# Kernel tuning notes

Measured on AMD Instinct MI355X. Metric: run time of the kernel, lower is better.

The kernel has to match this reference:

```python
import jax, jax.numpy as jnp
import numpy as np

IGNORE = 255
THRESH = 0.7
MIN_KEPT = 100000
AUX_W = 1.0


def resize_bilinear_ac(x, oh, ow):
    # F.interpolate(..., mode='bilinear', align_corners=True); x: (b,c,h,w)
    b, c, h, w = x.shape
    ys = jnp.linspace(0.0, h - 1.0, oh)
    xs = jnp.linspace(0.0, w - 1.0, ow)
    y0 = jnp.floor(ys).astype(jnp.int32)
    x0 = jnp.floor(xs).astype(jnp.int32)
    y1 = jnp.minimum(y0 + 1, h - 1)
    x1 = jnp.minimum(x0 + 1, w - 1)
    wy = (ys - y0)[:, None]          # (oh,1) broadcasts over (b,c,oh,w)
    wx = xs - x0                     # (ow,)
    rows = x[:, :, y0, :] * (1.0 - wy) + x[:, :, y1, :] * wy   # (b,c,oh,w)
    return rows[:, :, :, x0] * (1.0 - wx) + rows[:, :, :, x1] * wx


def ohem_ce(pred, target):
    # pred: (b,c,h,w) logits, target: (b,h,w) int labels
    b, c, h, w = pred.shape
    n = b * h * w
    t = target.reshape(-1)
    valid = t != IGNORE
    t_cl = jnp.where(valid, t, 0)
    logits = pred.transpose(0, 2, 3, 1).reshape(n, c)
    logp = jax.nn.log_softmax(logits, axis=-1)
    pix = jnp.arange(n)
    logp_t = logp[pix, t_cl]
    # prob at target class; invalid pixels filled with 1 (as in masked_fill_)
    mask_prob = jnp.where(valid, jnp.exp(logp_t), 1.0)
    idx = min(n, MIN_KEPT) - 1
    thr = jnp.maximum(jnp.asarray(THRESH, pred.dtype), jnp.sort(mask_prob)[idx])
    kept = mask_prob <= thr
    final_valid = valid & kept
    nll = -logp_t
    denom = jnp.maximum(final_valid.sum(), 1).astype(pred.dtype)
    return jnp.sum(jnp.where(final_valid, nll, 0.0)) / denom


def boundary_bce(p, t):
    # p: (n,1,h,w) probs, t: (n,1,h,w) binary targets; per-sample pos/neg weights
    pos = jnp.sum(t == 1.0, axis=(1, 2, 3), keepdims=True).astype(p.dtype)
    neg = jnp.sum(t == 0.0, axis=(1, 2, 3), keepdims=True).astype(p.dtype)
    valid = pos + neg
    wgt = jnp.where(t == 1.0, neg / valid, jnp.where(t == 0.0, pos / valid, 0.0))
    logp = jnp.clip(jnp.log(p), -100.0)          # torch BCELoss clamps log at -100
    log1mp = jnp.clip(jnp.log(1.0 - p), -100.0)
    bce = -(t * logp + (1.0 - t) * log1mp)
    return jnp.mean(wgt * bce)


def setup_inputs() -> dict:
    key = jax.random.key(0)
    k1, k2, k3, k4, k5 = jax.random.split(key, 5)
    main_pred = jax.random.normal(k1, (4, 19, 64, 128), dtype=jnp.float32)
    coarse_pred = jax.random.normal(k2, (4, 19, 64, 128), dtype=jnp.float32)
    boundary_pred = jax.random.uniform(k3, (4, 1, 64, 128), dtype=jnp.float32)
    seg_gt = jax.random.randint(k4, (4, 512, 1024), 0, 19, dtype=jnp.int32)
    boundary_gt = jax.random.randint(k5, (4, 1, 512, 1024), 0, 2).astype(jnp.float32)
    return {"main_pred": main_pred, "coarse_pred": coarse_pred,
            "boundary_pred": boundary_pred, "seg_gt": seg_gt,
            "boundary_gt": boundary_gt}


def reference(main_pred, coarse_pred, boundary_pred, seg_gt, boundary_gt):
    h, w = seg_gt.shape[1], seg_gt.shape[2]
    main_up = resize_bilinear_ac(main_pred, h, w)
    loss = ohem_ce(main_up, seg_gt)
    coarse_up = resize_bilinear_ac(coarse_pred, h, w)
    loss = loss + AUX_W * ohem_ce(coarse_up, seg_gt)
    bound_up = resize_bilinear_ac(boundary_pred, h, w)
    loss = loss + boundary_bce(bound_up, boundary_gt)
    return loss
```

## Files before the change

### kernel.cpp

```cpp
#include <hip/hip_runtime.h>

#define NPX    2097152
#define NPX4   (NPX/4)
#define CH_STR 8192
#define IMG_STR 155648

#define OFF_CTL   (2ull*NPX*4)
#define CTL_HIST    0
#define CTL_CNT1    0
#define CTL_CNT2    2048
#define CTL_BAR     24576
#define CTL_FLAG    24579
#define CTL_PREFIX  24580
#define CTL_KREM    24582
#define CTL_THR     24584
#define CTL_PPSUM   24586
#define CTL_PPCNT   28682
#define CTL_OPSUM   32778
#define CTL_OPCNT   33290
#define CTL_BPS     33802
#define CTL_BPC     34826

#define MAGIC_FAST 0x3A9C67E5u
#define GRID_P1    4608u

__device__ __forceinline__ void st_dev_f(float* p, float v) {
    __hip_atomic_store(p, v, __ATOMIC_RELAXED, __HIP_MEMORY_SCOPE_AGENT);
}
__device__ __forceinline__ void st_dev_u(unsigned* p, unsigned v) {
    __hip_atomic_store(p, v, __ATOMIC_RELAXED, __HIP_MEMORY_SCOPE_AGENT);
}
__device__ __forceinline__ float ld_dev_f(const float* p) {
    return __hip_atomic_load((float*)p, __ATOMIC_RELAXED, __HIP_MEMORY_SCOPE_AGENT);
}
__device__ __forceinline__ unsigned ld_dev_u(const unsigned* p) {
    return __hip_atomic_load((unsigned*)p, __ATOMIC_RELAXED, __HIP_MEMORY_SCOPE_AGENT);
}

__global__ __launch_bounds__(256) void fused_pass1(
    const float* __restrict__ mp, const float* __restrict__ cp,
    const float* __restrict__ bp, const int* __restrict__ seg,
    const float* __restrict__ bg,
    float* __restrict__ probA, float* __restrict__ ppsum, unsigned* __restrict__ ppcnt,
    float* __restrict__ bps, unsigned* __restrict__ bpc,
    unsigned* __restrict__ cnt1, unsigned* __restrict__ cnt2,
    unsigned* __restrict__ flag,
    float* __restrict__ out)
{
    __shared__ float2 erow[19 * 128];
    __shared__ float rf[4]; __shared__ unsigned ru[4];
    __shared__ float rf2[4]; __shared__ unsigned ru2[4];
    __shared__ unsigned amLast;
    __shared__ float Pb[4], Nb[4]; __shared__ unsigned PCb[4], NCb[4];
    int bk = blockIdx.x;
    int tid = threadIdx.x;

    if (bk < 4096) {
        int x = bk & 7, j = bk >> 3;
        int v = ((j >> 3) << 6) | (x << 3) | (j & 7);
        int head = v >> 11;
        int task = v & 2047;
        int b = task >> 9;
        int y = task & 511;
        const float* pred = head ? cp : mp;

        float fy = (float)y * (63.0f / 511.0f);
        int y0 = min((int)fy, 63);
        int y1 = min(y0 + 1, 63);
        float wy = fy - (float)y0;

        const float* r0 = pred + (size_t)b * IMG_STR + y0 * 128;
        const float* r1 = pred + (size_t)b * IMG_STR + y1 * 128;
        for (int i = tid; i < 2432; i += 256) {
            int c = i >> 7, xx = i & 127;
            float v0 = r0[c * CH_STR + xx];
            float v1 = r1[c * CH_STR + xx];
            float e = fmaf(wy, v1 - v0, v0);
            erow[c * 128 + xx].x = e;
            if (xx > 0)    erow[c * 128 + xx - 1].y = e;
            if (xx == 127) erow[c * 128 + 127].y = e;
        }
        __syncthreads();

        int xb = tid << 2;
        int P = (b * 512 + y) * 1024 + xb;
        int4 t4 = *(const int4*)(seg + P);
        int t[4] = {t4.x, t4.y, t4.z, t4.w};

        float fx0 = (float)xb * (127.0f / 1023.0f);
        int X = min((int)fx0, 126);
        float wA[4], wB[4], wC[4];
#pragma unroll
        for (int dx = 0; dx < 4; ++dx) {
            float fx = (float)(xb + dx) * (127.0f / 1023.0f);
            int x0 = min((int)fx, 127);
            float wx = fx - (float)x0;
            bool sm = (x0 == X);
            wA[dx] = sm ? (1.0f - wx) : 0.0f;
            wB[dx] = sm ? wx : (1.0f - wx);
            wC[dx] = sm ? 0.0f : wx;
        }

        float s[4] = {0.f, 0.f, 0.f, 0.f};
        for (int c = 0; c < 19; ++c) {
            float2 eA = erow[c * 128 + X];
            float2 eB = erow[c * 128 + X + 1];
#pragma unroll
            for (int dx = 0; dx < 4; ++dx) {
                float l = fmaf(eA.x, wA[dx], fmaf(eA.y, wB[dx], eB.y * wC[dx]));
                s[dx] += __expf(l);
            }
        }

        float fs = 0.f; unsigned ic = 0;
        float pr[4];
#pragma unroll
        for (int dx = 0; dx < 4; ++dx) {
            bool valid = (t[dx] != 255);
            int tc = valid ? t[dx] : 0;
            float2 eA = erow[tc * 128 + X];
            float2 eB = erow[tc * 128 + X + 1];
            float lt = fmaf(eA.x, wA[dx], fmaf(eA.y, wB[dx], eB.y * wC[dx]));
            float ls = __logf(s[dx]);
            float n  = ls - lt;
            float p  = fminf(__expf(-n), 1.0f);
            pr[dx] = valid ? p : 1.0f;
            if (valid && p <= 0.7f) { fs += n; ic++; }
        }
        *(float4*)(probA + (size_t)head * NPX + P) = make_float4(pr[0], pr[1], pr[2], pr[3]);

        for (int o = 32; o; o >>= 1) {
            fs += __shfl_down(fs, o, 64);
            ic += (unsigned)__shfl_down((int)ic, o, 64);
        }
        int wave = tid >> 6, lane = tid & 63;
        if (lane == 0) { rf[wave] = fs; ru[wave] = ic; }
        __syncthreads();
        if (tid == 0) {
            st_dev_f(&ppsum[head * 2048 + task], rf[0] + rf[1] + rf[2] + rf[3]);
            st_dev_u(&ppcnt[head * 2048 + task], ru[0] + ru[1] + ru[2] + ru[3]);
        }
    } else {
        int bb = bk - 4096;
        int b  = bb >> 7;
        int blk = bb & 127;
        float psum = 0.f, nsum = 0.f; unsigned pc = 0, nc = 0;

        for (int g = blk * 256 + tid; g < 131072; g += 128 * 256) {
            int P = g << 2;
            int y = P >> 10, xb = P & 1023;

            float fy = (float)y * (63.0f / 511.0f);
            int y0 = min((int)fy, 63);
            int y1 = min(y0 + 1, 63);
            float wy = fy - (float)y0;

            const float* r0 = bp + b * 8192 + y0 * 128;
            const float* r1 = bp + b * 8192 + y1 * 128;
            float fx0 = (float)xb * (127.0f / 1023.0f);
            int X  = min((int)fx0, 126);
            int X2 = min(X + 2, 127);
            float c0 = r0[X], c1 = r0[X + 1], c2 = r0[X2];
            float d0 = r1[X], d1 = r1[X + 1], d2 = r1[X2];
            float e0 = fmaf(wy, d0 - c0, c0);
            float e1 = fmaf(wy, d1 - c1, c1);
            float e2 = fmaf(wy, d2 - c2, c2);

            float4 t4 = *(const float4*)(bg + (size_t)b * 524288 + P);
            float tv[4] = {t4.x, t4.y, t4.z, t4.w};

#pragma unroll
            for (int dx = 0; dx < 4; ++dx) {
                float fx = (float)(xb + dx) * (127.0f / 1023.0f);
                int x0 = min((int)fx, 127);
                int x1 = min(x0 + 1, 127);
                float wx = fx - (float)x0;
                float a0 = (x0 == X)     ? e0 : e1;
                float a1 = (x1 == X + 1) ? e1 : e2;
                float p  = fmaf(wx, a1 - a0, a0);
                bool isp = (tv[dx] == 1.0f);
                bool isn = (tv[dx] == 0.0f);
                float q = isp ? p : 1.0f - p;
                float l = fmaxf(__logf(q), -100.0f);
                if (isp) { pc++; psum -= l; }
                if (isn) { nc++; nsum -= l; }
            }
        }
        for (int o = 32; o; o >>= 1) {
            psum += __shfl_down(psum, o, 64);
            nsum += __shfl_down(nsum, o, 64);
            pc   += (unsigned)__shfl_down((int)pc, o, 64);
            nc   += (unsigned)__shfl_down((int)nc, o, 64);
        }
        int wave = tid >> 6, lane = tid & 63;
        if (lane == 0) { rf[wave] = psum; rf2[wave] = nsum; ru[wave] = pc; ru2[wave] = nc; }
        __syncthreads();
        if (tid == 0) {
            st_dev_f(&bps[2 * bb],     rf[0] + rf[1] + rf[2] + rf[3]);
            st_dev_f(&bps[2 * bb + 1], rf2[0] + rf2[1] + rf2[2] + rf2[3]);
            st_dev_u(&bpc[2 * bb],     ru[0] + ru[1] + ru[2] + ru[3]);
            st_dev_u(&bpc[2 * bb + 1], ru2[0] + ru2[1] + ru2[2] + ru2[3]);
        }
    }

    __syncthreads();
    if (tid == 0) {
        asm volatile("s_waitcnt vmcnt(0)" ::: "memory");
        unsigned last = 0u;
        unsigned o1 = __hip_atomic_fetch_add(&cnt1[(bk & 63) << 5], 1u,
                                             __ATOMIC_RELAXED, __HIP_MEMORY_SCOPE_AGENT);
        if (o1 == 71u) {
            unsigned o2 = __hip_atomic_fetch_add(cnt2, 1u,
                                                 __ATOMIC_RELAXED, __HIP_MEMORY_SCOPE_AGENT);
            last = (o2 == 63u) ? 1u : 0u;
        }
        amLast = last;
    }
    __syncthreads();
    if (!amLast) return;

    float s0 = 0.f, s1 = 0.f; unsigned c0 = 0u, c1 = 0u;
    for (int i = tid; i < 2048; i += 256) {
        s0 += ld_dev_f(&ppsum[i]);        c0 += ld_dev_u(&ppcnt[i]);
        s1 += ld_dev_f(&ppsum[2048 + i]); c1 += ld_dev_u(&ppcnt[2048 + i]);
    }
    for (int o = 32; o; o >>= 1) {
        s0 += __shfl_down(s0, o, 64); s1 += __shfl_down(s1, o, 64);
        c0 += (unsigned)__shfl_down((int)c0, o, 64);
        c1 += (unsigned)__shfl_down((int)c1, o, 64);
    }
    int wv = tid >> 6, ln = tid & 63;
    if (ln == 0) { rf[wv] = s0; rf2[wv] = s1; ru[wv] = c0; ru2[wv] = c1; }
    __syncthreads();
    float S0 = rf[0] + rf[1] + rf[2] + rf[3];
    float S1 = rf2[0] + rf2[1] + rf2[2] + rf2[3];
    unsigned C0 = ru[0] + ru[1] + ru[2] + ru[3];
    unsigned C1 = ru2[0] + ru2[1] + ru2[2] + ru2[3];
    bool fast = (C0 >= 100000u) && (C1 >= 100000u);

    if (fast) {
        float*    lf = (float*)erow;
        unsigned* lu = (unsigned*)erow + 256;
        for (int b = 0; b < 4; ++b) {
            float ps = 0.f, ns = 0.f; unsigned p_c = 0, n_c = 0;
            if (tid < 128) {
                int jj = b * 128 + tid;
                ps  = ld_dev_f(&bps[2 * jj]); ns  = ld_dev_f(&bps[2 * jj + 1]);
                p_c = ld_dev_u(&bpc[2 * jj]); n_c = ld_dev_u(&bpc[2 * jj + 1]);
            }
            lf[tid] = ps; lu[tid] = p_c; __syncthreads();
            for (int o = 128; o; o >>= 1) {
                if (tid < o) { lf[tid] += lf[tid + o]; lu[tid] += lu[tid + o]; }
                __syncthreads();
            }
            if (tid == 0) { Pb[b] = lf[0]; PCb[b] = lu[0]; }
            __syncthreads();
            lf[tid] = ns; lu[tid] = n_c; __syncthreads();
            for (int o = 128; o; o >>= 1) {
                if (tid < o) { lf[tid] += lf[tid + o]; lu[tid] += lu[tid + o]; }
                __syncthreads();
            }
            if (tid == 0) { Nb[b] = lf[0]; NCb[b] = lu[0]; }
            __syncthreads();
        }
        if (tid == 0) {
            float bt = 0.f;
            for (int b = 0; b < 4; ++b) {
                float pos = (float)PCb[b], neg = (float)NCb[b];
                float val = fmaxf(pos + neg, 1.f);
                bt += (neg / val) * Pb[b] + (pos / val) * Nb[b];
            }
            float hls = S0 / fmaxf((float)C0, 1.f) + S1 / fmaxf((float)C1, 1.f);
            out[0] = hls + bt / 2097152.0f;
            st_dev_u(flag, MAGIC_FAST);
        }
    }
}

__device__ __forceinline__ void gbar(unsigned* bar, int tid) {
    __syncthreads();
    if (tid == 0) {
        unsigned g = __hip_atomic_load(&bar[1], __ATOMIC_RELAXED, __HIP_MEMORY_SCOPE_AGENT);
        unsigned t = __hip_atomic_fetch_add(&bar[0], 1u, __ATOMIC_ACQ_REL, __HIP_MEMORY_SCOPE_AGENT);
        if (t == 255u) {
            __hip_atomic_store(&bar[0], 0u, __ATOMIC_RELAXED, __HIP_MEMORY_SCOPE_AGENT);
            __hip_atomic_store(&bar[1], g + 1u, __ATOMIC_RELEASE, __HIP_MEMORY_SCOPE_AGENT);
        } else {
            while (__hip_atomic_load(&bar[1], __ATOMIC_ACQUIRE, __HIP_MEMORY_SCOPE_AGENT) == g)
                __builtin_amdgcn_s_sleep(8);
        }
    }
    __syncthreads();
}

__device__ void combine_out(int tid, float headLossSum,
                            const float* __restrict__ bps, const unsigned* __restrict__ bpc,
                            float* __restrict__ out)
{
    __shared__ float lf[256]; __shared__ unsigned lu[256];
    __shared__ float Pb[4], Nb[4]; __shared__ unsigned PCb[4], NCb[4];
    for (int b = 0; b < 4; ++b) {
        float ps = 0.f, ns = 0.f; unsigned p_c = 0, n_c = 0;
        if (tid < 128) {
            int j = b * 128 + tid;
            ps = bps[2 * j]; ns = bps[2 * j + 1];
            p_c = bpc[2 * j]; n_c = bpc[2 * j + 1];
        }
        lf[tid] = ps; lu[tid] = p_c; __syncthreads();
        for (int o = 128; o; o >>= 1) {
            if (tid < o) { lf[tid] += lf[tid + o]; lu[tid] += lu[tid + o]; }
            __syncthreads();
        }
        if (tid == 0) { Pb[b] = lf[0]; PCb[b] = lu[0]; }
        __syncthreads();
        lf[tid] = ns; lu[tid] = n_c; __syncthreads();
        for (int o = 128; o; o >>= 1) {
            if (tid < o) { lf[tid] += lf[tid + o]; lu[tid] += lu[tid + o]; }
            __syncthreads();
        }
        if (tid == 0) { Nb[b] = lf[0]; NCb[b] = lu[0]; }
        __syncthreads();
    }
    if (tid == 0) {
        float bt = 0.f;
        for (int b = 0; b < 4; ++b) {
            float pos = (float)PCb[b], neg = (float)NCb[b];
            float val = fmaxf(pos + neg, 1.f);
            bt += (neg / val) * Pb[b] + (pos / val) * Nb[b];
        }
        out[0] = headLossSum + bt / 2097152.0f;
    }
}

__global__ __launch_bounds__(256) void finish_all(
    const float* __restrict__ probA, const int* __restrict__ seg,
    const float* __restrict__ ppsum, const unsigned* __restrict__ ppcnt,
    const float* __restrict__ bps, const unsigned* __restrict__ bpc,
    unsigned* __restrict__ hist, unsigned* __restrict__ bar,
    unsigned* __restrict__ prefix, unsigned* __restrict__ krem,
    float* __restrict__ thr,
    float* __restrict__ opsum, unsigned* __restrict__ opcnt,
    unsigned* __restrict__ flag,
    float* __restrict__ out)
{
    if (*flag == MAGIC_FAST)
        return;

    int tid = threadIdx.x, blk = blockIdx.x;
    int wave = tid >> 6, lane = tid & 63;

    float s0 = 0.f, s1 = 0.f; unsigned c0 = 0u, c1 = 0u;
    for (int i = tid; i < 2048; i += 256) {
        s0 += ppsum[i];        c0 += ppcnt[i];
        s1 += ppsum[2048 + i]; c1 += ppcnt[2048 + i];
    }
    for (int o = 32; o; o >>= 1) {
        s0 += __shfl_down(s0, o, 64); s1 += __shfl_down(s1, o, 64);
        c0 += (unsigned)__shfl_down((int)c0, o, 64);
        c1 += (unsigned)__shfl_down((int)c1, o, 64);
    }
    __shared__ float ws0[4], ws1[4]; __shared__ unsigned wc0[4], wc1[4];
    if (lane == 0) { ws0[wave] = s0; ws1[wave] = s1; wc0[wave] = c0; wc1[wave] = c1; }
    __syncthreads();
    float S0 = ws0[0] + ws0[1] + ws0[2] + ws0[3];
    float S1 = ws1[0] + ws1[1] + ws1[2] + ws1[3];
    unsigned C0 = wc0[0] + wc0[1] + wc0[2] + wc0[3];
    unsigned C1 = wc1[0] + wc1[1] + wc1[2] + wc1[3];
    bool done0 = C0 >= 100000u, done1 = C1 >= 100000u;

    if (done0 && done1) {
        if (blk == 0)
            combine_out(tid, S0 / fmaxf((float)C0, 1.f) + S1 / fmaxf((float)C1, 1.f),
                        bps, bpc, out);
        return;
    }

    __shared__ unsigned hsh[4096];
    __shared__ unsigned cpre[257];
    unsigned doneMask = (done0 ? 1u : 0u) | (done1 ? 2u : 0u);

    for (int i = blk * 256 + tid; i < 24576; i += 65536) hist[i] = 0u;
    gbar(bar, tid);

    for (int lvl = 0; lvl < 3; ++lvl) {
        unsigned* hl = hist + lvl * 8192;
        for (int h = 0; h < 2; ++h) {
            if (doneMask & (1u << h)) continue;
            unsigned pre = (lvl == 0) ? 0u : prefix[h];
            for (int i = tid; i < 4096; i += 256) hsh[i] = 0u;
            __syncthreads();
            const float4* prob = (const float4*)(probA + (size_t)h * NPX);
            for (int i = blk * 256 + tid; i < NPX4; i += 65536) {
                float4 p = prob[i];
                unsigned u[4] = {__float_as_uint(p.x), __float_as_uint(p.y),
                                 __float_as_uint(p.z), __float_as_uint(p.w)};
#pragma unroll
                for (int k = 0; k < 4; ++k) {
                    unsigned bv = u[k];
                    if (lvl == 0)      atomicAdd(&hsh[bv >> 18], 1u);
                    else if (lvl == 1) { if ((bv >> 18) == pre) atomicAdd(&hsh[(bv >> 6) & 0xFFFu], 1u); }
                    else               { if ((bv >> 6) == pre) atomicAdd(&hsh[bv & 63u], 1u); }
                }
            }
            __syncthreads();
            for (int i = tid; i < 4096; i += 256) {
                unsigned v = hsh[i];
                if (v) atomicAdd(&hl[h * 4096 + i], v);
            }
            __syncthreads();
        }
        gbar(bar, tid);
        if (blk == 0) {
            int bins = (lvl == 2) ? 64 : 4096;
            for (int h = 0; h < 2; ++h) {
                if (doneMask & (1u << h)) continue;
                const unsigned* hh = hl + h * 4096;
                int per = (bins + 255) >> 8;
                int base = tid * per;
                unsigned ssum = 0;
                for (int i = 0; i < per; ++i) { int idx = base + i; if (idx < bins) ssum += hh[idx]; }
                cpre[tid] = ssum; __syncthreads();
                if (tid == 0) {
                    unsigned acc = 0;
                    for (int i = 0; i < 256; ++i) { unsigned v = cpre[i]; cpre[i] = acc; acc += v; }
                    cpre[256] = acc;
                }
                __syncthreads();
                unsigned K = (lvl == 0) ? 100000u : krem[h];
                unsigned my = cpre[tid], nx = cpre[tid + 1];
                if (K > 0 && my < K && K <= nx) {
                    unsigned acc = my;
                    for (int i = 0; i < per; ++i) {
                        int idx = base + i;
                        unsigned c = (idx < bins) ? hh[idx] : 0u;
                        if (acc < K && K <= acc + c) {
                            if (lvl == 0)      { prefix[h] = (unsigned)idx; krem[h] = K - acc; }
                            else if (lvl == 1) { prefix[h] = (prefix[h] << 12) | (unsigned)idx; krem[h] = K - acc; }
                            else {
                                unsigned bitsv = (prefix[h] << 6) | (unsigned)idx;
                                thr[h] = fmaxf(0.7f, __uint_as_float(bitsv));
                            }
                            break;
                        }
                        acc += c;
                    }
                }
                __syncthreads();
            }
        }
        gbar(bar, tid);
    }

    for (int h = 0; h < 2; ++h) {
        if (doneMask & (1u << h)) continue;
        float th = thr[h];
        const float4* prob = (const float4*)(probA + (size_t)h * NPX);
        const int4*   sg4  = (const int4*)seg;
        float fs = 0.f; unsigned ic = 0;
        for (int i = blk * 256 + tid; i < NPX4; i += 65536) {
            float4 p = prob[i]; int4 tt = sg4[i];
            if (tt.x != 255 && p.x <= th) { fs -= __logf(p.x); ic++; }
            if (tt.y != 255 && p.y <= th) { fs -= __logf(p.y); ic++; }
            if (tt.z != 255 && p.z <= th) { fs -= __logf(p.z); ic++; }
            if (tt.w != 255 && p.w <= th) { fs -= __logf(p.w); ic++; }
        }
        for (int o = 32; o; o >>= 1) {
            fs += __shfl_down(fs, o, 64);
            ic += (unsigned)__shfl_down((int)ic, o, 64);
        }
        __shared__ float wf[4]; __shared__ unsigned wu[4];
        if (lane == 0) { wf[wave] = fs; wu[wave] = ic; }
        __syncthreads();
        if (tid == 0) {
            opsum[h * 256 + blk] = wf[0] + wf[1] + wf[2] + wf[3];
            opcnt[h * 256 + blk] = wu[0] + wu[1] + wu[2] + wu[3];
        }
        __syncthreads();
    }
    gbar(bar, tid);
    if (blk == 0) {
        __shared__ float lf2[256]; __shared__ unsigned lu2[256];
        float hls = 0.f;
        for (int h = 0; h < 2; ++h) {
            float S; unsigned C;
            if (doneMask & (1u << h)) {
                S = h ? S1 : S0; C = h ? C1 : C0;
            } else {
                lf2[tid] = opsum[h * 256 + tid]; lu2[tid] = opcnt[h * 256 + tid];
                __syncthreads();
                for (int o = 128; o; o >>= 1) {
                    if (tid < o) { lf2[tid] += lf2[tid + o]; lu2[tid] += lu2[tid + o]; }
                    __syncthreads();
                }
                S = lf2[0]; C = lu2[0];
                __syncthreads();
            }
            hls += S / fmaxf((float)C, 1.f);
        }
        combine_out(tid, hls, bps, bpc, out);
    }
}

extern "C" void kernel_launch(void* const* d_in, const int* in_sizes, int n_in,
                              void* d_out, int out_size, void* d_ws, size_t ws_size,
                              hipStream_t stream)
{
    const float* mp  = (const float*)d_in[0];
    const float* cp  = (const float*)d_in[1];
    const float* bp  = (const float*)d_in[2];
    const int*   seg = (const int*)d_in[3];
    const float* bg  = (const float*)d_in[4];
    float* out = (float*)d_out;

    char* ws = (char*)d_ws;
    float* probA = (float*)ws;
    unsigned* ctl    = (unsigned*)(ws + OFF_CTL);
    unsigned* hist   = ctl + CTL_HIST;
    unsigned* cnt1   = ctl + CTL_CNT1;
    unsigned* cnt2   = ctl + CTL_CNT2;
    unsigned* bar    = ctl + CTL_BAR;
    unsigned* flag   = ctl + CTL_FLAG;
    unsigned* prefix = ctl + CTL_PREFIX;
    unsigned* krem   = ctl + CTL_KREM;
    float*    thr    = (float*)(ctl + CTL_THR);
    float*    ppsum  = (float*)(ctl + CTL_PPSUM);
    unsigned* ppcnt  = ctl + CTL_PPCNT;
    float*    opsum  = (float*)(ctl + CTL_OPSUM);
    unsigned* opcnt  = ctl + CTL_OPCNT;
    float*    bps    = (float*)(ctl + CTL_BPS);
    unsigned* bpc    = ctl + CTL_BPC;

    hipMemsetAsync(ws + OFF_CTL, 0, 24580ull * 4, stream);

    fused_pass1<<<dim3(GRID_P1), 256, 0, stream>>>(mp, cp, bp, seg, bg, probA,
                                                   ppsum, ppcnt, bps, bpc,
                                                   cnt1, cnt2, flag, out);
    finish_all<<<dim3(256), 256, 0, stream>>>(probA, seg, ppsum, ppcnt, bps, bpc,
                                              hist, bar, prefix, krem, thr,
                                              opsum, opcnt, flag, out);
}
```

Baseline: 113.3 us.

## Process four output rows per block, reusing three loaded source rows in registers

Each segmentation block now handles four consecutive output rows instead of one. It loads the three source rows those rows can span once into registers as float4 vectors, then builds the per-row interpolated shared buffer with shuffles and vector stores. This cuts redundant global loads of source rows and block launch overhead, and shrinks the pass-1 grid, so the last-block counter threshold is adjusted to match. The cost is more registers (launch bounds now request 5 blocks), fewer blocks in flight, and extra syncthreads per row.

Result: no change. 113.1 us (-0.2%).

```diff
diff --git a/kernel.cpp b/kernel.cpp
--- a/kernel.cpp
+++ b/kernel.cpp
@@ -22,7 +22,7 @@
 #define CTL_BPC     34826
 
 #define MAGIC_FAST 0x3A9C67E5u
-#define GRID_P1    4608u
+#define GRID_P1    1536u
 
 __device__ __forceinline__ void st_dev_f(float* p, float v) {
     __hip_atomic_store(p, v, __ATOMIC_RELAXED, __HIP_MEMORY_SCOPE_AGENT);
@@ -37,7 +37,7 @@
     return __hip_atomic_load((unsigned*)p, __ATOMIC_RELAXED, __HIP_MEMORY_SCOPE_AGENT);
 }
 
-__global__ __launch_bounds__(256) void fused_pass1(
+__global__ __launch_bounds__(256, 5) void fused_pass1(
     const float* __restrict__ mp, const float* __restrict__ cp,
     const float* __restrict__ bp, const int* __restrict__ seg,
     const float* __restrict__ bg,
@@ -55,38 +55,34 @@
     int bk = blockIdx.x;
     int tid = threadIdx.x;
 
-    if (bk < 4096) {
-        int x = bk & 7, j = bk >> 3;
-        int v = ((j >> 3) << 6) | (x << 3) | (j & 7);
-        int head = v >> 11;
-        int task = v & 2047;
-        int b = task >> 9;
-        int y = task & 511;
+    if (bk < 1024) {
+        int v = ((bk & 7) << 7) | (bk >> 3);
+        int head = v >> 9;
+        int b    = (v >> 7) & 3;
+        int k    = v & 127;
         const float* pred = head ? cp : mp;
 
-        float fy = (float)y * (63.0f / 511.0f);
-        int y0 = min((int)fy, 63);
-        int y1 = min(y0 + 1, 63);
-        float wy = fy - (float)y0;
-
-        const float* r0 = pred + (size_t)b * IMG_STR + y0 * 128;
-        const float* r1 = pred + (size_t)b * IMG_STR + y1 * 128;
-        for (int i = tid; i < 2432; i += 256) {
-            int c = i >> 7, xx = i & 127;
-            float v0 = r0[c * CH_STR + xx];
-            float v1 = r1[c * CH_STR + xx];
-            float e = fmaf(wy, v1 - v0, v0);
-            erow[c * 128 + xx].x = e;
-            if (xx > 0)    erow[c * 128 + xx - 1].y = e;
-            if (xx == 127) erow[c * 128 + 127].y = e;
-        }
-        __syncthreads();
+        int y0g = min((int)((float)(4 * k) * (63.0f / 511.0f)), 63);
+        int row0 = y0g, row1 = min(y0g + 1, 63), row2 = min(y0g + 2, 63);
+
+        float4 rv[3][3];
+#pragma unroll
+        for (int r = 0; r < 3; ++r) {
+            int ry = (r == 0) ? row0 : ((r == 1) ? row1 : row2);
+            const float* rp = pred + (size_t)b * IMG_STR + ry * 128;
+#pragma unroll
+            for (int sr = 0; sr < 3; ++sr) {
+                int s = tid + (sr << 8);
+                if (s < 608) {
+                    int c = s >> 5, x4 = (s & 31) << 2;
+                    rv[r][sr] = *(const float4*)(rp + c * CH_STR + x4);
+                } else {
+                    rv[r][sr] = make_float4(0.f, 0.f, 0.f, 0.f);
+                }
+            }
+        }
 
         int xb = tid << 2;
-        int P = (b * 512 + y) * 1024 + xb;
-        int4 t4 = *(const int4*)(seg + P);
-        int t[4] = {t4.x, t4.y, t4.z, t4.w};
-
         float fx0 = (float)xb * (127.0f / 1023.0f);
         int X = min((int)fx0, 126);
         float wA[4], wB[4], wC[4];
@@ -101,47 +97,82 @@
             wC[dx] = sm ? 0.0f : wx;
         }
 
-        float s[4] = {0.f, 0.f, 0.f, 0.f};
-        for (int c = 0; c < 19; ++c) {
-            float2 eA = erow[c * 128 + X];
-            float2 eB = erow[c * 128 + X + 1];
+#pragma unroll 1
+        for (int d = 0; d < 4; ++d) {
+            int y = (k << 2) + d;
+            int task = (b << 9) + y;
+            float fy = (float)y * (63.0f / 511.0f);
+            int y0 = min((int)fy, 63);
+            float wy = fy - (float)y0;
+            int j = y0 - y0g;
+
+            int P = task * 1024 + xb;
+            int4 t4 = *(const int4*)(seg + P);
+            int t[4] = {t4.x, t4.y, t4.z, t4.w};
+
+#pragma unroll
+            for (int sr = 0; sr < 3; ++sr) {
+                int s = tid + (sr << 8);
+                float4 cu = (j == 0) ? rv[0][sr] : rv[1][sr];
+                float4 nx = (j == 0) ? rv[1][sr] : rv[2][sr];
+                float e0 = fmaf(wy, nx.x - cu.x, cu.x);
+                float e1 = fmaf(wy, nx.y - cu.y, cu.y);
+                float e2 = fmaf(wy, nx.z - cu.z, cu.z);
+                float e3 = fmaf(wy, nx.w - cu.w, cu.w);
+                float en = __shfl_down(e0, 1, 64);
+                if (s < 608) {
+                    int c = s >> 5, x4 = (s & 31) << 2;
+                    float last = ((s & 31) == 31) ? e3 : en;
+                    float4 w0 = make_float4(e0, e1, e1, e2);
+                    float4 w1 = make_float4(e2, e3, e3, last);
+                    *(float4*)(&erow[c * 128 + x4])     = w0;
+                    *(float4*)(&erow[c * 128 + x4 + 2]) = w1;
+                }
+            }
+            __syncthreads();
+
+            float acc[4] = {0.f, 0.f, 0.f, 0.f};
+            for (int c = 0; c < 19; ++c) {
+                float2 eA = erow[c * 128 + X];
+                float2 eB = erow[c * 128 + X + 1];
+#pragma unroll
+                for (int dx = 0; dx < 4; ++dx) {
+                    float l = fmaf(eA.x, wA[dx], fmaf(eA.y, wB[dx], eB.y * wC[dx]));
+                    acc[dx] += __expf(l);
+                }
+            }
+
+            float fs = 0.f; unsigned ic = 0;
+            float pr[4];
 #pragma unroll
             for (int dx = 0; dx < 4; ++dx) {
-                float l = fmaf(eA.x, wA[dx], fmaf(eA.y, wB[dx], eB.y * wC[dx]));
-                s[dx] += __expf(l);
-            }
-        }
-
-        float fs = 0.f; unsigned ic = 0;
-        float pr[4];
-#pragma unroll
-        for (int dx = 0; dx < 4; ++dx) {
-            bool valid = (t[dx] != 255);
-            int tc = valid ? t[dx] : 0;
-            float2 eA = erow[tc * 128 + X];
-            float2 eB = erow[tc * 128 + X + 1];
-            float lt = fmaf(eA.x, wA[dx], fmaf(eA.y, wB[dx], eB.y * wC[dx]));
-            float ls = __logf(s[dx]);
-            float n  = ls - lt;
-            float p  = fminf(__expf(-n), 1.0f);
-            pr[dx] = valid ? p : 1.0f;
-            if (valid && p <= 0.7f) { fs += n; ic++; }
-        }
-        *(float4*)(probA + (size_t)head * NPX + P) = make_float4(pr[0], pr[1], pr[2], pr[3]);
-
-        for (int o = 32; o; o >>= 1) {
-            fs += __shfl_down(fs, o, 64);
-            ic += (unsigned)__shfl_down((int)ic, o, 64);
-        }
-        int wave = tid >> 6, lane = tid & 63;
-        if (lane == 0) { rf[wave] = fs; ru[wave] = ic; }
-        __syncthreads();
-        if (tid == 0) {
-            st_dev_f(&ppsum[head * 2048 + task], rf[0] + rf[1] + rf[2] + rf[3]);
-            st_dev_u(&ppcnt[head * 2048 + task], ru[0] + ru[1] + ru[2] + ru[3]);
+                bool valid = (t[dx] != 255);
+                int tc = valid ? t[dx] : 0;
+                float2 eA = erow[tc * 128 + X];
+                float2 eB = erow[tc * 128 + X + 1];
+                float lt = fmaf(eA.x, wA[dx], fmaf(eA.y, wB[dx], eB.y * wC[dx]));
+                float ls = __logf(acc[dx]);
+                float n  = ls - lt;
+                float p  = fminf(__expf(-n), 1.0f);
+                pr[dx] = valid ? p : 1.0f;
+                if (valid && p <= 0.7f) { fs += n; ic++; }
+            }
+            *(float4*)(probA + (size_t)head * NPX + P) = make_float4(pr[0], pr[1], pr[2], pr[3]);
+
+            for (int o = 32; o; o >>= 1) {
+                fs += __shfl_down(fs, o, 64);
+                ic += (unsigned)__shfl_down((int)ic, o, 64);
+            }
+            int wave = tid >> 6, lane = tid & 63;
+            if (lane == 0) { rf[wave] = fs; ru[wave] = ic; }
+            __syncthreads();
+            if (tid == 0) {
+                st_dev_f(&ppsum[head * 2048 + task], rf[0] + rf[1] + rf[2] + rf[3]);
+                st_dev_u(&ppcnt[head * 2048 + task], ru[0] + ru[1] + ru[2] + ru[3]);
+            }
         }
     } else {
-        int bb = bk - 4096;
+        int bb = bk - 1024;
         int b  = bb >> 7;
         int blk = bb & 127;
         float psum = 0.f, nsum = 0.f; unsigned pc = 0, nc = 0;
@@ -209,7 +240,7 @@
         unsigned last = 0u;
         unsigned o1 = __hip_atomic_fetch_add(&cnt1[(bk & 63) << 5], 1u,
                                              __ATOMIC_RELAXED, __HIP_MEMORY_SCOPE_AGENT);
-        if (o1 == 71u) {
+        if (o1 == 23u) {
             unsigned o2 = __hip_atomic_fetch_add(cnt2, 1u,
                                                  __ATOMIC_RELAXED, __HIP_MEMORY_SCOPE_AGENT);
             last = (o2 == 63u) ? 1u : 0u;
@@ -395,8 +426,8 @@
                 unsigned u[4] = {__float_as_uint(p.x), __float_as_uint(p.y),
                                  __float_as_uint(p.z), __float_as_uint(p.w)};
 #pragma unroll
-                for (int k = 0; k < 4; ++k) {
-                    unsigned bv = u[k];
+                for (int kk = 0; kk < 4; ++kk) {
+                    unsigned bv = u[kk];
                     if (lvl == 0)      atomicAdd(&hsh[bv >> 18], 1u);
                     else if (lvl == 1) { if ((bv >> 18) == pre) atomicAdd(&hsh[(bv >> 6) & 0xFFFu], 1u); }
                     else               { if ((bv >> 6) == pre) atomicAdd(&hsh[bv & 63u], 1u); }
```
